# Optimization experiments

Measured on AMD Instinct MI355X. Metric: run time of the kernel, lower is better.

## Reference

```python
import jax, jax.numpy as jnp
import numpy as np

DIM = 512
D_STATE = 16
D_CONV = 4
EXPAND = 2
D_INNER = EXPAND * DIM          # 1024
DT_RANK = (DIM + D_STATE - 1) // D_STATE  # 32
B_SZ, L_SEQ = 2, 2048


def layer_norm(x, w, b, eps=1e-5):
    mu = jnp.mean(x, axis=-1, keepdims=True)
    var = jnp.mean(jnp.square(x - mu), axis=-1, keepdims=True)
    return (x - mu) * jax.lax.rsqrt(var + eps) * w + b


def setup_inputs() -> dict:
    key = jax.random.key(0)
    ks = jax.random.split(key, 12)
    x = jax.random.normal(ks[0], (B_SZ, DIM, L_SEQ), dtype=jnp.float32)
    # LayerNorms init to weight=1, bias=0 per _init_weights
    norm1_w = jnp.ones((DIM,), jnp.float32)
    norm1_b = jnp.zeros((DIM,), jnp.float32)
    norm2_w = jnp.ones((DIM,), jnp.float32)
    norm2_b = jnp.zeros((DIM,), jnp.float32)
    # Mamba params (Linear weights trunc-normal std=0.02 per _init_weights; bias=0)
    in_proj_w = 0.02 * jax.random.truncated_normal(ks[1], -2., 2., (2 * D_INNER, DIM), jnp.float32)
    conv_w = 0.1 * jax.random.normal(ks[2], (D_INNER, D_CONV), jnp.float32)
    conv_b = jnp.zeros((D_INNER,), jnp.float32)
    x_proj_w = 0.02 * jax.random.truncated_normal(ks[3], -2., 2., (DT_RANK + 2 * D_STATE, D_INNER), jnp.float32)
    dt_proj_w = 0.02 * jax.random.truncated_normal(ks[4], -2., 2., (D_INNER, DT_RANK), jnp.float32)
    # dt bias: inverse-softplus of dt ~ U(1e-3, 0.1), standard Mamba init
    dt = jnp.exp(jax.random.uniform(ks[5], (D_INNER,), jnp.float32) * (np.log(0.1) - np.log(1e-3)) + np.log(1e-3))
    dt_proj_b = dt + jnp.log(-jnp.expm1(-dt))
    # S4D-real init: A = diag(1..d_state), stored as log
    A_log = jnp.log(jnp.broadcast_to(jnp.arange(1, D_STATE + 1, dtype=jnp.float32), (D_INNER, D_STATE)))
    D = jnp.ones((D_INNER,), jnp.float32)
    out_proj_w = 0.02 * jax.random.truncated_normal(ks[6], -2., 2., (DIM, D_INNER), jnp.float32)
    return {"x": x, "norm1_w": norm1_w, "norm1_b": norm1_b, "norm2_w": norm2_w,
            "norm2_b": norm2_b, "in_proj_w": in_proj_w, "conv_w": conv_w, "conv_b": conv_b,
            "x_proj_w": x_proj_w, "dt_proj_w": dt_proj_w, "dt_proj_b": dt_proj_b,
            "A_log": A_log, "D": D, "out_proj_w": out_proj_w}


def mamba_block(xn, in_proj_w, conv_w, conv_b, x_proj_w, dt_proj_w, dt_proj_b, A_log, D, out_proj_w):
    # xn: [B, L, dim]
    Bb, Ll, _ = xn.shape
    di = in_proj_w.shape[0] // 2
    xz = jnp.einsum('bld,ed->ble', xn, in_proj_w)          # [B, L, 2*di]
    x_in, z = xz[..., :di], xz[..., di:]
    # depthwise causal conv1d over L
    K = conv_w.shape[1]
    xp = jnp.pad(x_in, ((0, 0), (K - 1, 0), (0, 0)))
    xc = sum(xp[:, k:k + Ll, :] * conv_w[:, k] for k in range(K)) + conv_b
    xc = jax.nn.silu(xc)                                    # [B, L, di]
    # input-dependent dt, B, C
    dbl = jnp.einsum('bld,ed->ble', xc, x_proj_w)
    R, N = dt_proj_w.shape[1], A_log.shape[1]
    dt_lo, Bm, Cm = dbl[..., :R], dbl[..., R:R + N], dbl[..., R + N:]
    dt = jax.nn.softplus(jnp.einsum('blr,dr->bld', dt_lo, dt_proj_w) + dt_proj_b)  # [B, L, di]
    A = -jnp.exp(A_log)                                     # [di, N]
    dA = jnp.exp(jnp.einsum('bld,dn->bldn', dt, A))         # [B, L, di, N]
    dBu = jnp.einsum('bld,bln,bld->bldn', dt, Bm, xc)       # dt * B * u
    def step(h, inp):
        dA_t, dBu_t, C_t = inp                              # [B,di,N], [B,di,N], [B,N]
        h = dA_t * h + dBu_t
        y = jnp.einsum('bdn,bn->bd', h, C_t)
        return h, y
    h0 = jnp.zeros((Bb, di, N), xn.dtype)
    _, ys = jax.lax.scan(step, h0, (jnp.swapaxes(dA, 0, 1), jnp.swapaxes(dBu, 0, 1), jnp.swapaxes(Cm, 0, 1)))
    y = jnp.swapaxes(ys, 0, 1)                              # [B, L, di]
    y = y + xc * D
    y = y * jax.nn.silu(z)
    return jnp.einsum('ble,de->bld', y, out_proj_w)         # [B, L, dim]


def reference(x, norm1_w, norm1_b, norm2_w, norm2_b, in_proj_w, conv_w, conv_b,
              x_proj_w, dt_proj_w, dt_proj_b, A_log, D, out_proj_w):
    # x: [B, C, L]
    xf = jnp.swapaxes(x, 1, 2)                              # [B, L, C]
    xn = layer_norm(xf, norm1_w, norm1_b)
    xm = mamba_block(xn, in_proj_w, conv_w, conv_b, x_proj_w,
                     dt_proj_w, dt_proj_b, A_log, D, out_proj_w)
    out = layer_norm(xf + xm, norm2_w, norm2_b)
    return jnp.swapaxes(out, 1, 2)                          # [B, C, L]
```

## Files before the change

### kernel.cpp

```cpp
#include <hip/hip_runtime.h>
#include <math.h>

#define BSZ 2
#define LSEQ 2048
#define DMODEL 512
#define DINNER 1024
#define NST 16
#define RDT 32
#define GDBL 64
#define NCH 32
#define CHL 64
#define LOG2E 1.4426950408889634f

typedef unsigned short u16;
typedef unsigned int   u32;
typedef __attribute__((ext_vector_type(8))) __bf16 bf16x8;
typedef __attribute__((ext_vector_type(4))) float  f32x4;

__device__ __forceinline__ float siluf(float x){ return x / (1.f + __expf(-x)); }
__device__ __forceinline__ float softplusf(float x){
  return (x > 20.f) ? x : log1pf(__expf(x));
}
__device__ __forceinline__ u16 f2bf(float f){
  u32 u = __float_as_uint(f);
  u += 0x7fff + ((u >> 16) & 1);
  return (u16)(u >> 16);
}
__device__ __forceinline__ float bf2f(u16 u){ return __uint_as_float((u32)u << 16); }
__device__ __forceinline__ float exp2fast(float x){
  float r; asm("v_exp_f32 %0, %1" : "=v"(r) : "v"(x)); return r;
}
__device__ __forceinline__ void gld16(const void* g, void* l){
  __builtin_amdgcn_global_load_lds((const __attribute__((address_space(1))) void*)g,
                                   (__attribute__((address_space(3))) void*)l, 16, 0, 0);
}
__device__ __forceinline__ void unpack8(uint4 v, float* f){
  f[0]=__uint_as_float(v.x<<16); f[1]=__uint_as_float(v.x&0xffff0000u);
  f[2]=__uint_as_float(v.y<<16); f[3]=__uint_as_float(v.y&0xffff0000u);
  f[4]=__uint_as_float(v.z<<16); f[5]=__uint_as_float(v.z&0xffff0000u);
  f[6]=__uint_as_float(v.w<<16); f[7]=__uint_as_float(v.w&0xffff0000u);
}
__device__ __forceinline__ float quadsum(float p){
  p += __int_as_float(__builtin_amdgcn_update_dpp(0, __float_as_int(p), 0xB1, 0xf, 0xf, true));
  p += __int_as_float(__builtin_amdgcn_update_dpp(0, __float_as_int(p), 0x4E, 0xf, 0xf, true));
  return p;
}

__global__ void k01_wcvt_ln(const float* __restrict__ Wip, const float* __restrict__ Wop,
                            const float* __restrict__ Wxp, const float* __restrict__ Wdt,
                            u16* __restrict__ wipb, u16* __restrict__ wopb,
                            u16* __restrict__ wxpb, u16* __restrict__ wdtb,
                            const float* __restrict__ x, const float* __restrict__ w1,
                            const float* __restrict__ b1, u16* __restrict__ xnb){
  __shared__ float ss[8][33], qq[8][33];
  __shared__ float muL[32], rsL[32];
  if (blockIdx.x < 1632){
    int idx = blockIdx.x*256 + threadIdx.x;
    int i4 = idx * 4;
    const float* src; u16* dst;
    if (i4 < 1048576){ src = Wip + i4; dst = wipb + i4; }
    else if (i4 < 1048576 + 524288){ int j = i4 - 1048576; src = Wop + j; dst = wopb + j; }
    else if (i4 < 1048576 + 524288 + 65536){ int j = i4 - 1048576 - 524288; src = Wxp + j; dst = wxpb + j; }
    else { int j = i4 - 1048576 - 524288 - 65536; if (j >= 32768) return; src = Wdt + j; dst = wdtb + j; }
    float4 v = *(const float4*)src;
    u32 lo = (u32)f2bf(v.x) | ((u32)f2bf(v.y) << 16);
    u32 hi = (u32)f2bf(v.z) | ((u32)f2bf(v.w) << 16);
    *(uint2*)dst = make_uint2(lo, hi);
    return;
  }
  int blk = blockIdx.x - 1632;
  int b = blk >> 6;
  int l0 = (blk & 63) * 32;
  int t = threadIdx.x;
  int lc = t & 31, dc = t >> 5;
  const float* xb = x + (size_t)b*DMODEL*LSEQ;
  float s=0.f, q=0.f;
  for (int d = dc*64; d < dc*64+64; ++d){
    float v = xb[d*LSEQ + l0 + lc];
    s += v; q += v*v;
  }
  ss[dc][lc]=s; qq[dc][lc]=q;
  __syncthreads();
  if (t < 32){
    float S=0.f,Q=0.f;
    for (int i=0;i<8;++i){S+=ss[i][t];Q+=qq[i][t];}
    float m = S/DMODEL;
    muL[t]=m; rsL[t]=rsqrtf(Q/DMODEL - m*m + 1e-5f);
  }
  __syncthreads();
  float mu = muL[lc], rs = rsL[lc];
  u16* orow = xnb + ((size_t)(b*LSEQ + l0 + lc))*DMODEL;
  for (int d = dc*64; d < dc*64+64; d += 2){
    float v0 = (xb[d*LSEQ + l0 + lc]     - mu)*rs*w1[d]   + b1[d];
    float v1 = (xb[(d+1)*LSEQ + l0 + lc] - mu)*rs*w1[d+1] + b1[d+1];
    *(u32*)&orow[d] = (u32)f2bf(v0) | ((u32)f2bf(v1) << 16);
  }
}

__global__ __launch_bounds__(256) void k2_inproj_mfma(
    const u16* __restrict__ xnb, const u16* __restrict__ wipb,
    u16* __restrict__ xinb, u16* __restrict__ zb){
  __shared__ u16 As[2][4096];
  __shared__ u16 Bs[2][4096];
  int t = threadIdx.x;
  int wid = t >> 6, lane = t & 63;
  int n0 = blockIdx.x * 128, m0 = blockIdx.y * 128;
  int wr = wid >> 1, wc = wid & 1;
  int lr = lane & 15, q = lane >> 4;

  const u16* gA = xnb  + (size_t)(m0 + (t>>2))*DMODEL + (t&3)*8;
  const u16* gB = wipb + (size_t)(n0 + (t>>2))*DMODEL + (t&3)*8;

  f32x4 acc[4][4];
  #pragma unroll
  for (int i=0;i<4;++i)
    #pragma unroll
    for (int j=0;j<4;++j) acc[i][j] = (f32x4){0.f,0.f,0.f,0.f};

  #pragma unroll
  for (int r=0;r<2;++r){
    gld16(gA + (size_t)r*64*DMODEL, &As[0][(wid*64 + r*256)*8]);
    gld16(gB + (size_t)r*64*DMODEL, &Bs[0][(wid*64 + r*256)*8]);
  }
  const int abase = (wr*64 + lr)*32 + q*8;
  const int bbase = (wc*64 + lr)*32 + q*8;

  for (int ks = 0; ks < 16; ++ks){
    int cur = ks & 1;
    __syncthreads();
    if (ks < 15){
      const u16* gA2 = gA + (ks+1)*32;
      const u16* gB2 = gB + (ks+1)*32;
      #pragma unroll
      for (int r=0;r<2;++r){
        gld16(gA2 + (size_t)r*64*DMODEL, &As[cur^1][(wid*64 + r*256)*8]);
        gld16(gB2 + (size_t)r*64*DMODEL, &Bs[cur^1][(wid*64 + r*256)*8]);
      }
    }
    bf16x8 a[4], bv[4];
    #pragma unroll
    for (int mf=0; mf<4; ++mf) a[mf]  = *(const bf16x8*)&As[cur][abase + mf*512];
    #pragma unroll
    for (int nf=0; nf<4; ++nf) bv[nf] = *(const bf16x8*)&Bs[cur][bbase + nf*512];
    #pragma unroll
    for (int mf=0; mf<4; ++mf)
      #pragma unroll
      for (int nf=0; nf<4; ++nf)
        acc[mf][nf] = __builtin_amdgcn_mfma_f32_16x16x32_bf16(a[mf], bv[nf], acc[mf][nf], 0, 0, 0);
  }

  bool half = (n0 >= DINNER);
  u16* outp = half ? zb : xinb;
  int colb = (half ? n0 - DINNER : n0) + wc*64 + lr;
  #pragma unroll
  for (int mf=0; mf<4; ++mf){
    int rowb = m0 + wr*64 + mf*16 + q*4;
    #pragma unroll
    for (int nf=0; nf<4; ++nf){
      f32x4 v = acc[mf][nf];
      int col = colb + nf*16;
      #pragma unroll
      for (int j=0;j<4;++j) outp[(size_t)(rowb+j)*DINNER + col] = f2bf(v[j]);
    }
  }
}

__global__ void k3_conv(const u16* __restrict__ xinb, const float* __restrict__ cw,
                        const float* __restrict__ cb, u16* __restrict__ xc){
  int idx = blockIdx.x*blockDim.x + threadIdx.x;
  int e4 = (idx & (DINNER/4 - 1)) * 4;
  int m = idx >> 8;
  int b = m >> 11; int l = m & (LSEQ-1);
  float4 accb = *(const float4*)&cb[e4];
  float acc[4] = {accb.x, accb.y, accb.z, accb.w};
  #pragma unroll
  for (int k=0;k<4;++k){
    int li = l + k - 3;
    if (li >= 0){
      ushort4 v = *(const ushort4*)&xinb[((size_t)(b*LSEQ+li))*DINNER + e4];
      acc[0] += bf2f(v.x) * cw[(e4+0)*4 + k];
      acc[1] += bf2f(v.y) * cw[(e4+1)*4 + k];
      acc[2] += bf2f(v.z) * cw[(e4+2)*4 + k];
      acc[3] += bf2f(v.w) * cw[(e4+3)*4 + k];
    }
  }
  u32 lo = (u32)f2bf(siluf(acc[0])) | ((u32)f2bf(siluf(acc[1])) << 16);
  u32 hi = (u32)f2bf(siluf(acc[2])) | ((u32)f2bf(siluf(acc[3])) << 16);
  *(uint2*)&xc[(size_t)m*DINNER + e4] = make_uint2(lo, hi);
}

__global__ __launch_bounds__(256) void k4_xproj_mfma(
    const u16* __restrict__ xcbf, const u16* __restrict__ wxpb,
    float* __restrict__ dbl, u16* __restrict__ dtlob){
  __shared__ u16 As[2][4096];
  __shared__ u16 Bs[2][4096];
  int t = threadIdx.x;
  int wid = t >> 6, lane = t & 63;
  int m0 = blockIdx.x * 64;
  int wr = wid >> 1, wc = wid & 1;
  int lr = lane & 15, q = lane >> 4;

  const u16* gA = xcbf + (size_t)(m0 + (t>>2))*DINNER + (t&3)*8;
  const u16* gB = wxpb + (size_t)(t>>2)*DINNER + (t&3)*8;

  f32x4 acc[2][2];
  #pragma unroll
  for (int i=0;i<2;++i)
    #pragma unroll
    for (int j=0;j<2;++j) acc[i][j] = (f32x4){0.f,0.f,0.f,0.f};

  #pragma unroll
  for (int r=0;r<2;++r){
    gld16(gA + r*32, &As[0][(r*256 + wid*64)*8]);
    gld16(gB + r*32, &Bs[0][(r*256 + wid*64)*8]);
  }
  const int abase = (wr*32 + lr)*32 + q*8;
  const int bbase = (wc*32 + lr)*32 + q*8;

  for (int ks = 0; ks < 16; ++ks){
    int cur = ks & 1;
    __syncthreads();
    if (ks < 15){
      const u16* gA2 = gA + (ks+1)*64;
      const u16* gB2 = gB + (ks+1)*64;
      #pragma unroll
      for (int r=0;r<2;++r){
        gld16(gA2 + r*32, &As[cur^1][(r*256 + wid*64)*8]);
        gld16(gB2 + r*32, &Bs[cur^1][(r*256 + wid*64)*8]);
      }
    }
    bf16x8 a[2][2], bv[2][2];
    #pragma unroll
    for (int mf=0; mf<2; ++mf)
      #pragma unroll
      for (int s=0; s<2; ++s) a[mf][s] = *(const bf16x8*)&As[cur][abase + mf*512 + s*2048];
    #pragma unroll
    for (int nf=0; nf<2; ++nf)
      #pragma unroll
      for (int s=0; s<2; ++s) bv[nf][s] = *(const bf16x8*)&Bs[cur][bbase + nf*512 + s*2048];
    #pragma unroll
    for (int s=0; s<2; ++s)
      #pragma unroll
      for (int mf=0; mf<2; ++mf)
        #pragma unroll
        for (int nf=0; nf<2; ++nf)
          acc[mf][nf] = __builtin_amdgcn_mfma_f32_16x16x32_bf16(a[mf][s], bv[nf][s], acc[mf][nf], 0, 0, 0);
  }

  #pragma unroll
  for (int mf=0; mf<2; ++mf){
    int rowb = m0 + wr*32 + mf*16 + q*4;
    #pragma unroll
    for (int nf=0; nf<2; ++nf){
      f32x4 v = acc[mf][nf];
      int col = wc*32 + nf*16 + lr;
      #pragma unroll
      for (int j=0;j<4;++j) dbl[(size_t)(rowb+j)*GDBL + col] = v[j];
      if (wc == 0){
        #pragma unroll
        for (int j=0;j<4;++j) dtlob[(size_t)(rowb+j)*RDT + col] = f2bf(v[j]);
      }
    }
  }
}

__global__ __launch_bounds__(256) void k5_dtproj_mfma(
    const u16* __restrict__ dtlob, const u16* __restrict__ wdtb,
    const float* __restrict__ dtbias, u16* __restrict__ dtb){
  __shared__ u16 As[2048];
  __shared__ u16 Bs[2048];
  int t = threadIdx.x;
  int wid = t >> 6, lane = t & 63;
  int m0 = blockIdx.x * 64, d0 = blockIdx.y * 64;
  int wr = wid >> 1, wc = wid & 1;
  int lr = lane & 15, q = lane >> 4;

  gld16(dtlob + (size_t)(m0 + (t>>2))*RDT + (t&3)*8, &As[wid*512]);
  gld16(wdtb  + (size_t)(d0 + (t>>2))*RDT + (t&3)*8, &Bs[wid*512]);
  __syncthreads();

  f32x4 acc[2][2];
  bf16x8 a[2], bv[2];
  #pragma unroll
  for (int mf=0; mf<2; ++mf) a[mf]  = *(const bf16x8*)&As[(wr*32 + mf*16 + lr)*32 + q*8];
  #pragma unroll
  for (int nf=0; nf<2; ++nf) bv[nf] = *(const bf16x8*)&Bs[(wc*32 + nf*16 + lr)*32 + q*8];
  #pragma unroll
  for (int mf=0; mf<2; ++mf)
    #pragma unroll
    for (int nf=0; nf<2; ++nf)
      acc[mf][nf] = __builtin_amdgcn_mfma_f32_16x16x32_bf16(a[mf], bv[nf], (f32x4){0.f,0.f,0.f,0.f}, 0, 0, 0);

  #pragma unroll
  for (int nf=0; nf<2; ++nf){
    int col = d0 + wc*32 + nf*16 + lr;
    float bias = dtbias[col];
    #pragma unroll
    for (int mf=0; mf<2; ++mf){
      int rowb = m0 + wr*32 + mf*16 + q*4;
      f32x4 v = acc[mf][nf];
      #pragma unroll
      for (int j=0;j<4;++j) dtb[(size_t)(rowb+j)*DINNER + col] = f2bf(softplusf(v[j] + bias));
    }
  }
}

__global__ __launch_bounds__(256) void k6a_pass1(
    const float* __restrict__ dblg, const u16* __restrict__ xcg, const u16* __restrict__ dtg,
    const float* __restrict__ Alog,
    float* __restrict__ hend, float* __restrict__ dchunk){
  int blk = blockIdx.x;
  int b = blk >> 9;
  int dblk = (blk >> 5) & 15;
  int chunk = blk & 31;
  int d0 = dblk * 64;
  int t = threadIdx.x;
  int d = t >> 2, ng = t & 3;

  float4 Adn2;
  {
    float4 al = *(const float4*)&Alog[(d0+d)*NST + ng*4];
    Adn2.x = -__expf(al.x)*LOG2E; Adn2.y = -__expf(al.y)*LOG2E;
    Adn2.z = -__expf(al.z)*LOG2E; Adn2.w = -__expf(al.w)*LOG2E;
  }
  float h0=0.f, h1=0.f, h2=0.f, h3=0.f, S=0.f;

  __shared__ float dts[32][64];
  __shared__ float xcs[32][64];
  __shared__ float Bst[32][16];

  for (int sub = 0; sub < CHL/32; ++sub){
    int l0 = chunk*CHL + sub*32;
    __syncthreads();
    {
      int r = t >> 3, c8 = t & 7;
      size_t row = (size_t)(b*LSEQ + l0 + r);
      uint4 dv = *(const uint4*)&dtg[row*DINNER + d0 + c8*8];
      uint4 xv = *(const uint4*)&xcg[row*DINNER + d0 + c8*8];
      float df[8], xf[8];
      unpack8(dv, df); unpack8(xv, xf);
      *(float4*)&dts[r][c8*8]   = make_float4(df[0],df[1],df[2],df[3]);
      *(float4*)&dts[r][c8*8+4] = make_float4(df[4],df[5],df[6],df[7]);
      *(float4*)&xcs[r][c8*8]   = make_float4(xf[0],xf[1],xf[2],xf[3]);
      *(float4*)&xcs[r][c8*8+4] = make_float4(xf[4],xf[5],xf[6],xf[7]);
      if (t < 128){
        int rB = t >> 2, qB = t & 3;
        *(float4*)&Bst[rB][qB*4] = *(const float4*)&dblg[((size_t)(b*LSEQ + l0 + rB))*GDBL + RDT + qB*4];
      }
    }
    __syncthreads();
    #pragma unroll 4
    for (int r = 0; r < 32; ++r){
      float dtv = dts[r][d];
      float xcv = xcs[r][d];
      float4 Bv = *(const float4*)&Bst[r][ng*4];
      float u = dtv * xcv;
      h0 = exp2fast(dtv*Adn2.x)*h0 + u*Bv.x;
      h1 = exp2fast(dtv*Adn2.y)*h1 + u*Bv.y;
      h2 = exp2fast(dtv*Adn2.z)*h2 + u*Bv.z;
      h3 = exp2fast(dtv*Adn2.w)*h3 + u*Bv.w;
      S += dtv;
    }
  }
  size_t cix = ((size_t)(b*NCH + chunk)*DINNER + d0 + d)*NST + ng*4;
  *(float4*)&hend[cix]   = make_float4(h0, h1, h2, h3);
  *(float4*)&dchunk[cix] = make_float4(exp2fast(Adn2.x*S), exp2fast(Adn2.y*S),
                                       exp2fast(Adn2.z*S), exp2fast(Adn2.w*S));
}

__global__ __launch_bounds__(256) void k6c_pass2(
    const float* __restrict__ dblg, const u16* __restrict__ xcg, const u16* __restrict__ zg,
    const u16* __restrict__ dtg,
    const float* __restrict__ Alog, const float* __restrict__ Dp,
    const float* __restrict__ hend, const float* __restrict__ dchk,
    u16* __restrict__ ybf){
  int blk = blockIdx.x;
  int b = blk >> 9;
  int dblk = (blk >> 5) & 15;
  int chunk = blk & 31;
  int d0 = dblk * 64;
  int t = threadIdx.x;
  int d = t >> 2, ng = t & 3;

  float4 Adn2;
  {
    float4 al = *(const float4*)&Alog[(d0+d)*NST + ng*4];
    Adn2.x = -__expf(al.x)*LOG2E; Adn2.y = -__expf(al.y)*LOG2E;
    Adn2.z = -__expf(al.z)*LOG2E; Adn2.w = -__expf(al.w)*LOG2E;
  }

  float h0=0.f, h1=0.f, h2=0.f, h3=0.f;
  {
    size_t base = ((size_t)(b*NCH)*DINNER + d0 + d)*NST + ng*4;
    for (int c = 0; c < chunk; ++c){
      size_t ix = base + (size_t)c*DINNER*NST;
      float4 hv = *(const float4*)&hend[ix];
      float4 dv = *(const float4*)&dchk[ix];
      h0 = dv.x*h0 + hv.x; h1 = dv.y*h1 + hv.y;
      h2 = dv.z*h2 + hv.z; h3 = dv.w*h3 + hv.w;
    }
  }

  __shared__ float dts[32][64];
  __shared__ float xcs[32][64];
  __shared__ float BCs[32][32];
  __shared__ float ys[32][64];
  __shared__ float Dps[64];

  if (t < 64) Dps[t] = Dp[d0 + t];

  for (int sub = 0; sub < CHL/32; ++sub){
    int l0 = chunk*CHL + sub*32;
    __syncthreads();
    {
      int r = t >> 3, c8 = t & 7;
      size_t row = (size_t)(b*LSEQ + l0 + r);
      uint4 dv = *(const uint4*)&dtg[row*DINNER + d0 + c8*8];
      uint4 xv = *(const uint4*)&xcg[row*DINNER + d0 + c8*8];
      float df[8], xf[8];
      unpack8(dv, df); unpack8(xv, xf);
      *(float4*)&dts[r][c8*8]   = make_float4(df[0],df[1],df[2],df[3]);
      *(float4*)&dts[r][c8*8+4] = make_float4(df[4],df[5],df[6],df[7]);
      *(float4*)&xcs[r][c8*8]   = make_float4(xf[0],xf[1],xf[2],xf[3]);
      *(float4*)&xcs[r][c8*8+4] = make_float4(xf[4],xf[5],xf[6],xf[7]);
      *(float4*)&BCs[r][c8*4]   = *(const float4*)&dblg[row*GDBL + RDT + c8*4];
    }
    __syncthreads();
    #pragma unroll 4
    for (int r = 0; r < 32; ++r){
      float dtv = dts[r][d];
      float xcv = xcs[r][d];
      float4 Bv = *(const float4*)&BCs[r][ng*4];
      float4 Cv = *(const float4*)&BCs[r][16 + ng*4];
      float u = dtv * xcv;
      h0 = exp2fast(dtv*Adn2.x)*h0 + u*Bv.x;
      h1 = exp2fast(dtv*Adn2.y)*h1 + u*Bv.y;
      h2 = exp2fast(dtv*Adn2.z)*h2 + u*Bv.z;
      h3 = exp2fast(dtv*Adn2.w)*h3 + u*Bv.w;
      float p = h0*Cv.x + h1*Cv.y + h2*Cv.z + h3*Cv.w;
      p = quadsum(p);
      if (ng == 0) ys[r][d] = p;
    }
    __syncthreads();
    {
      int r = t >> 3, c8 = t & 7;
      size_t row = (size_t)(b*LSEQ + l0 + r);
      uint4 zv = *(const uint4*)&zg[row*DINNER + d0 + c8*8];
      float zf[8]; unpack8(zv, zf);
      float4 s0 = *(const float4*)&ys[r][c8*8];
      float4 s1 = *(const float4*)&ys[r][c8*8+4];
      float4 x0 = *(const float4*)&xcs[r][c8*8];
      float4 x1 = *(const float4*)&xcs[r][c8*8+4];
      float4 D0 = *(const float4*)&Dps[c8*8];
      float4 D1 = *(const float4*)&Dps[c8*8+4];
      float y0 = (s0.x + x0.x*D0.x)*siluf(zf[0]);
      float y1 = (s0.y + x0.y*D0.y)*siluf(zf[1]);
      float y2 = (s0.z + x0.z*D0.z)*siluf(zf[2]);
      float y3 = (s0.w + x0.w*D0.w)*siluf(zf[3]);
      float y4 = (s1.x + x1.x*D1.x)*siluf(zf[4]);
      float y5 = (s1.y + x1.y*D1.y)*siluf(zf[5]);
      float y6 = (s1.z + x1.z*D1.z)*siluf(zf[6]);
      float y7 = (s1.w + x1.w*D1.w)*siluf(zf[7]);
      uint4 o;
      o.x = (u32)f2bf(y0) | ((u32)f2bf(y1) << 16);
      o.y = (u32)f2bf(y2) | ((u32)f2bf(y3) << 16);
      o.z = (u32)f2bf(y4) | ((u32)f2bf(y5) << 16);
      o.w = (u32)f2bf(y6) | ((u32)f2bf(y7) << 16);
      *(uint4*)&ybf[row*DINNER + d0 + c8*8] = o;
    }
  }
}

__global__ __launch_bounds__(256) void k7_outproj_mfma(
    const u16* __restrict__ ybf, const u16* __restrict__ wopb, u16* __restrict__ xmTb){
  __shared__ u16 As[2][4096];
  __shared__ u16 Bs[2][4096];
  int t = threadIdx.x;
  int wid = t >> 6, lane = t & 63;
  int n0 = blockIdx.x * 64, m0 = blockIdx.y * 64;
  int b  = m0 >> 11;
  int l0 = m0 & (LSEQ-1);
  int wr = wid >> 1, wc = wid & 1;
  int lr = lane & 15, q = lane >> 4;

  const u16* gA = ybf  + (size_t)(m0 + (t>>2))*DINNER + (t&3)*8;
  const u16* gB = wopb + (size_t)(n0 + (t>>2))*DINNER + (t&3)*8;

  f32x4 acc[2][2];
  #pragma unroll
  for (int i=0;i<2;++i)
    #pragma unroll
    for (int j=0;j<2;++j) acc[i][j] = (f32x4){0.f,0.f,0.f,0.f};

  #pragma unroll
  for (int r=0;r<2;++r){
    gld16(gA + r*32, &As[0][(r*256 + wid*64)*8]);
    gld16(gB + r*32, &Bs[0][(r*256 + wid*64)*8]);
  }
  const int abase = (wr*32 + lr)*32 + q*8;
  const int bbase = (wc*32 + lr)*32 + q*8;

  for (int ks = 0; ks < 16; ++ks){
    int cur = ks & 1;
    __syncthreads();
    if (ks < 15){
      const u16* gA2 = gA + (ks+1)*64;
      const u16* gB2 = gB + (ks+1)*64;
      #pragma unroll
      for (int r=0;r<2;++r){
        gld16(gA2 + r*32, &As[cur^1][(r*256 + wid*64)*8]);
        gld16(gB2 + r*32, &Bs[cur^1][(r*256 + wid*64)*8]);
      }
    }
    bf16x8 a[2][2], bv[2][2];
    #pragma unroll
    for (int mf=0; mf<2; ++mf)
      #pragma unroll
      for (int s=0; s<2; ++s) a[mf][s] = *(const bf16x8*)&As[cur][abase + mf*512 + s*2048];
    #pragma unroll
    for (int nf=0; nf<2; ++nf)
      #pragma unroll
      for (int s=0; s<2; ++s) bv[nf][s] = *(const bf16x8*)&Bs[cur][bbase + nf*512 + s*2048];
    #pragma unroll
    for (int s=0; s<2; ++s)
      #pragma unroll
      for (int mf=0; mf<2; ++mf)
        #pragma unroll
        for (int nf=0; nf<2; ++nf)
          acc[mf][nf] = __builtin_amdgcn_mfma_f32_16x16x32_bf16(a[mf][s], bv[nf][s], acc[mf][nf], 0, 0, 0);
  }

  #pragma unroll
  for (int mf=0; mf<2; ++mf){
    int lrow = l0 + wr*32 + mf*16 + q*4;
    #pragma unroll
    for (int nf=0; nf<2; ++nf){
      f32x4 v = acc[mf][nf];
      int col = n0 + wc*32 + nf*16 + lr;
      u32 lo = (u32)f2bf(v[0]) | ((u32)f2bf(v[1]) << 16);
      u32 hi = (u32)f2bf(v[2]) | ((u32)f2bf(v[3]) << 16);
      *(uint2*)&xmTb[((size_t)(b*DMODEL + col))*LSEQ + lrow] = make_uint2(lo, hi);
    }
  }
}

__global__ void k8_fused(const float* __restrict__ x, const u16* __restrict__ xmTb,
                         const float* __restrict__ w2, const float* __restrict__ b2,
                         float* __restrict__ out){
  int blk = blockIdx.x;
  int b = blk >> 7;
  int l0 = (blk & 127) * 16;
  int t = threadIdx.x;
  int lc = t & 15, dc = t >> 4;
  const float* xb = x    + (size_t)b*DMODEL*LSEQ + l0 + lc;
  const u16*   xt = xmTb + (size_t)b*DMODEL*LSEQ + l0 + lc;
  float s=0.f, q=0.f;
  for (int d = dc*32; d < dc*32+32; ++d){
    float v = xb[d*LSEQ] + bf2f(xt[d*LSEQ]);
    s += v; q += v*v;
  }
  __shared__ float ss[16][17], qq[16][17];
  __shared__ float muL[16], rsL[16];
  ss[dc][lc]=s; qq[dc][lc]=q;
  __syncthreads();
  if (t < 16){
    float S=0.f,Q=0.f;
    for (int i=0;i<16;++i){S+=ss[i][t];Q+=qq[i][t];}
    float m = S/DMODEL;
    muL[t]=m; rsL[t]=rsqrtf(Q/DMODEL - m*m + 1e-5f);
  }
  __syncthreads();
  float mu = muL[lc], rs = rsL[lc];
  float* ob = out + (size_t)b*DMODEL*LSEQ + l0 + lc;
  for (int d = dc*32; d < dc*32+32; ++d){
    float v = xb[d*LSEQ] + bf2f(xt[d*LSEQ]);
    ob[d*LSEQ] = (v - mu)*rs*w2[d] + b2[d];
  }
}

extern "C" void kernel_launch(void* const* d_in, const int* in_sizes, int n_in,
                              void* d_out, int out_size, void* d_ws, size_t ws_size,
                              hipStream_t stream) {
  const float* x      = (const float*)d_in[0];
  const float* n1w    = (const float*)d_in[1];
  const float* n1b    = (const float*)d_in[2];
  const float* n2w    = (const float*)d_in[3];
  const float* n2b    = (const float*)d_in[4];
  const float* Wip    = (const float*)d_in[5];
  const float* cw     = (const float*)d_in[6];
  const float* cb     = (const float*)d_in[7];
  const float* Wxp    = (const float*)d_in[8];
  const float* Wdt    = (const float*)d_in[9];
  const float* dtbias = (const float*)d_in[10];
  const float* Alog   = (const float*)d_in[11];
  const float* Dp     = (const float*)d_in[12];
  const float* Wop    = (const float*)d_in[13];
  float* out = (float*)d_out;

  float* ws = (float*)d_ws;
  size_t o = 0;
  u16*  xinb = (u16*)(ws + o); o += 2097152;
  u16*  zb   = (u16*)(ws + o); o += 2097152;
  u16*  xcb  = (u16*)(ws + o); o += 2097152;
  u16*  ybf  = (u16*)(ws + o); o += 2097152;
  u16*  dtb  = (u16*)(ws + o); o += 2097152;
  u16*  xnb  = (u16*)(ws + o); o += 1048576;
  u16*  wipb = (u16*)(ws + o); o += 524288;
  u16*  wopb = (u16*)(ws + o); o += 262144;
  u16*  wxpb = (u16*)(ws + o); o += 32768;
  u16*  wdtb = (u16*)(ws + o); o += 16384;
  u16*  dtlob= (u16*)(ws + o); o += 65536;
  float* dbl  = ws + o; o += 262144;
  float* hend = ws + o; o += 1048576;
  float* dchk = ws + o; o += 1048576;
  u16*  xmTb  = (u16*)(ws + o); o += 1048576;

  k01_wcvt_ln  <<<dim3(1760),        dim3(256), 0, stream>>>(Wip, Wop, Wxp, Wdt, wipb, wopb, wxpb, wdtb,
                                                             x, n1w, n1b, xnb);
  k2_inproj_mfma<<<dim3(16,32),      dim3(256), 0, stream>>>(xnb, wipb, xinb, zb);
  k3_conv      <<<dim3(4096),        dim3(256), 0, stream>>>(xinb, cw, cb, xcb);
  k4_xproj_mfma<<<dim3(64),          dim3(256), 0, stream>>>(xcb, wxpb, dbl, dtlob);
  k5_dtproj_mfma<<<dim3(64,16),      dim3(256), 0, stream>>>(dtlob, wdtb, dtbias, dtb);
  k6a_pass1    <<<dim3(BSZ*16*NCH),  dim3(256), 0, stream>>>(dbl, xcb, dtb, Alog, hend, dchk);
  k6c_pass2    <<<dim3(BSZ*16*NCH),  dim3(256), 0, stream>>>(dbl, xcb, zb, dtb, Alog, Dp, hend, dchk, ybf);
  k7_outproj_mfma<<<dim3(8,64),      dim3(256), 0, stream>>>(ybf, wopb, xmTb);
  k8_fused     <<<dim3(BSZ*128),     dim3(256), 0, stream>>>(x, xmTb, n2w, n2b, out);
}
```

Baseline: 160.4 us.

## Fuse dt projection into x_proj kernel and use fast silu/softplus intrinsics

Merges the dt_proj GEMM and its softplus into the x_proj kernel. The low-rank dt slice stays in shared memory and is multiplied against the dt weights in eight column chunks, which removes one launch and the dtlob round trip through global memory. The dt_proj work now runs on only 64 blocks instead of 1024, so parallelism drops for that stage. silu and softplus also switch to raw v_exp/v_log/v_rcp hardware approximations.

Result: no change. 162.8 us (+1.5%).

```diff
diff --git a/kernel.cpp b/kernel.cpp
--- a/kernel.cpp
+++ b/kernel.cpp
@@ -11,16 +11,13 @@
 #define NCH 32
 #define CHL 64
 #define LOG2E 1.4426950408889634f
+#define LN2   0.6931471805599453f
 
 typedef unsigned short u16;
 typedef unsigned int   u32;
 typedef __attribute__((ext_vector_type(8))) __bf16 bf16x8;
 typedef __attribute__((ext_vector_type(4))) float  f32x4;
 
-__device__ __forceinline__ float siluf(float x){ return x / (1.f + __expf(-x)); }
-__device__ __forceinline__ float softplusf(float x){
-  return (x > 20.f) ? x : log1pf(__expf(x));
-}
 __device__ __forceinline__ u16 f2bf(float f){
   u32 u = __float_as_uint(f);
   u += 0x7fff + ((u >> 16) & 1);
@@ -29,6 +26,19 @@
 __device__ __forceinline__ float bf2f(u16 u){ return __uint_as_float((u32)u << 16); }
 __device__ __forceinline__ float exp2fast(float x){
   float r; asm("v_exp_f32 %0, %1" : "=v"(r) : "v"(x)); return r;
+}
+__device__ __forceinline__ float log2fast(float x){
+  float r; asm("v_log_f32 %0, %1" : "=v"(r) : "v"(x)); return r;
+}
+__device__ __forceinline__ float rcpfast(float x){
+  float r; asm("v_rcp_f32 %0, %1" : "=v"(r) : "v"(x)); return r;
+}
+__device__ __forceinline__ float siluf(float x){
+  return x * rcpfast(1.f + exp2fast(-x*LOG2E));
+}
+__device__ __forceinline__ float softplusf(float x){
+  if (x > 20.f) return x;
+  return log2fast(1.f + exp2fast(x*LOG2E)) * LN2;
 }
 __device__ __forceinline__ void gld16(const void* g, void* l){
   __builtin_amdgcn_global_load_lds((const __attribute__((address_space(1))) void*)g,
@@ -189,9 +199,10 @@
   *(uint2*)&xc[(size_t)m*DINNER + e4] = make_uint2(lo, hi);
 }
 
-__global__ __launch_bounds__(256) void k4_xproj_mfma(
+__global__ __launch_bounds__(256) void k4_xproj_dt_mfma(
     const u16* __restrict__ xcbf, const u16* __restrict__ wxpb,
-    float* __restrict__ dbl, u16* __restrict__ dtlob){
+    const u16* __restrict__ wdtb, const float* __restrict__ dtbias,
+    float* __restrict__ dbl, u16* __restrict__ dtb){
   __shared__ u16 As[2][4096];
   __shared__ u16 Bs[2][4096];
   int t = threadIdx.x;
@@ -247,60 +258,50 @@
           acc[mf][nf] = __builtin_amdgcn_mfma_f32_16x16x32_bf16(a[mf][s], bv[nf][s], acc[mf][nf], 0, 0, 0);
   }
 
+  u16* dtlo_s = &As[0][0];
+  u16* wdt_s  = &Bs[0][0];
+  __syncthreads();
   #pragma unroll
   for (int mf=0; mf<2; ++mf){
     int rowb = m0 + wr*32 + mf*16 + q*4;
+    int rloc = wr*32 + mf*16 + q*4;
     #pragma unroll
     for (int nf=0; nf<2; ++nf){
       f32x4 v = acc[mf][nf];
       int col = wc*32 + nf*16 + lr;
-      #pragma unroll
-      for (int j=0;j<4;++j) dbl[(size_t)(rowb+j)*GDBL + col] = v[j];
-      if (wc == 0){
+      if (wc == 1){
         #pragma unroll
-        for (int j=0;j<4;++j) dtlob[(size_t)(rowb+j)*RDT + col] = f2bf(v[j]);
+        for (int j=0;j<4;++j) dbl[(size_t)(rowb+j)*GDBL + col] = v[j];
+      } else {
+        #pragma unroll
+        for (int j=0;j<4;++j) dtlo_s[(rloc+j)*32 + col] = f2bf(v[j]);
       }
     }
   }
-}
-
-__global__ __launch_bounds__(256) void k5_dtproj_mfma(
-    const u16* __restrict__ dtlob, const u16* __restrict__ wdtb,
-    const float* __restrict__ dtbias, u16* __restrict__ dtb){
-  __shared__ u16 As[2048];
-  __shared__ u16 Bs[2048];
-  int t = threadIdx.x;
-  int wid = t >> 6, lane = t & 63;
-  int m0 = blockIdx.x * 64, d0 = blockIdx.y * 64;
-  int wr = wid >> 1, wc = wid & 1;
-  int lr = lane & 15, q = lane >> 4;
-
-  gld16(dtlob + (size_t)(m0 + (t>>2))*RDT + (t&3)*8, &As[wid*512]);
-  gld16(wdtb  + (size_t)(d0 + (t>>2))*RDT + (t&3)*8, &Bs[wid*512]);
   __syncthreads();
-
-  f32x4 acc[2][2];
-  bf16x8 a[2], bv[2];
-  #pragma unroll
-  for (int mf=0; mf<2; ++mf) a[mf]  = *(const bf16x8*)&As[(wr*32 + mf*16 + lr)*32 + q*8];
-  #pragma unroll
-  for (int nf=0; nf<2; ++nf) bv[nf] = *(const bf16x8*)&Bs[(wc*32 + nf*16 + lr)*32 + q*8];
-  #pragma unroll
-  for (int mf=0; mf<2; ++mf)
-    #pragma unroll
-    for (int nf=0; nf<2; ++nf)
-      acc[mf][nf] = __builtin_amdgcn_mfma_f32_16x16x32_bf16(a[mf], bv[nf], (f32x4){0.f,0.f,0.f,0.f}, 0, 0, 0);
-
-  #pragma unroll
-  for (int nf=0; nf<2; ++nf){
-    int col = d0 + wc*32 + nf*16 + lr;
-    float bias = dtbias[col];
-    #pragma unroll
-    for (int mf=0; mf<2; ++mf){
-      int rowb = m0 + wr*32 + mf*16 + q*4;
-      f32x4 v = acc[mf][nf];
-      #pragma unroll
-      for (int j=0;j<4;++j) dtb[(size_t)(rowb+j)*DINNER + col] = f2bf(softplusf(v[j] + bias));
+  bf16x8 da[4];
+  #pragma unroll
+  for (int mf=0; mf<4; ++mf) da[mf] = *(const bf16x8*)&dtlo_s[(mf*16 + lr)*32 + q*8];
+  for (int c = 0; c < 8; ++c){
+    __syncthreads();
+    #pragma unroll
+    for (int r2=0; r2<2; ++r2)
+      gld16(wdtb + (size_t)(c*128 + r2*64 + (t>>2))*RDT + (t&3)*8, &wdt_s[r2*2048 + (t>>6)*512]);
+    __syncthreads();
+    bf16x8 db[2];
+    #pragma unroll
+    for (int nf=0; nf<2; ++nf) db[nf] = *(const bf16x8*)&wdt_s[(wid*32 + nf*16 + lr)*32 + q*8];
+    #pragma unroll
+    for (int nf=0; nf<2; ++nf){
+      int col = c*128 + wid*32 + nf*16 + lr;
+      float bias = dtbias[col];
+      #pragma unroll
+      for (int mf=0; mf<4; ++mf){
+        f32x4 v = __builtin_amdgcn_mfma_f32_16x16x32_bf16(da[mf], db[nf], (f32x4){0.f,0.f,0.f,0.f}, 0, 0, 0);
+        int rowb = m0 + mf*16 + q*4;
+        #pragma unroll
+        for (int j=0;j<4;++j) dtb[(size_t)(rowb+j)*DINNER + col] = f2bf(softplusf(v[j] + bias));
+      }
     }
   }
 }
@@ -609,7 +610,6 @@
   u16*  wopb = (u16*)(ws + o); o += 262144;
   u16*  wxpb = (u16*)(ws + o); o += 32768;
   u16*  wdtb = (u16*)(ws + o); o += 16384;
-  u16*  dtlob= (u16*)(ws + o); o += 65536;
   float* dbl  = ws + o; o += 262144;
   float* hend = ws + o; o += 1048576;
   float* dchk = ws + o; o += 1048576;
@@ -619,8 +619,7 @@
                                                              x, n1w, n1b, xnb);
   k2_inproj_mfma<<<dim3(16,32),      dim3(256), 0, stream>>>(xnb, wipb, xinb, zb);
   k3_conv      <<<dim3(4096),        dim3(256), 0, stream>>>(xinb, cw, cb, xcb);
-  k4_xproj_mfma<<<dim3(64),          dim3(256), 0, stream>>>(xcb, wxpb, dbl, dtlob);
-  k5_dtproj_mfma<<<dim3(64,16),      dim3(256), 0, stream>>>(dtlob, wdtb, dtbias, dtb);
+  k4_xproj_dt_mfma<<<dim3(64),       dim3(256), 0, stream>>>(xcb, wxpb, wdtb, dtbias, dbl, dtb);
   k6a_pass1    <<<dim3(BSZ*16*NCH),  dim3(256), 0, stream>>>(dbl, xcb, dtb, Alog, hend, dchk);
   k6c_pass2    <<<dim3(BSZ*16*NCH),  dim3(256), 0, stream>>>(dbl, xcb, zb, dtb, Alog, Dp, hend, dchk, ybf);
   k7_outproj_mfma<<<dim3(8,64),      dim3(256), 0, stream>>>(ybf, wopb, xmTb);
```
